# Kernel optimization log

Hardware: AMD Instinct MI355X
Metric: run time of the kernel (lower is better)

The kernel has to match this reference:

```python
import jax, jax.numpy as jnp
import numpy as np

EPS_RMS = 1e-6
EPS_NORM = 1e-9


def rmsnorm(x):
    return x * jax.lax.rsqrt(jnp.mean(x * x, axis=-1, keepdims=True) + EPS_RMS)


def apply_rotary(x, cos, sin):
    # x: [b, h, s, d]; cos/sin: [1, 1, s, d//2]
    d2 = x.shape[-1] // 2
    x1, x2 = x[..., :d2], x[..., d2:]
    return jnp.concatenate([x1 * cos - x2 * sin, x1 * sin + x2 * cos], axis=-1)


def setup_inputs() -> dict:
    key = jax.random.key(0)
    ks = jax.random.split(key, 16)
    b, l, e, h = 4, 1024, 2048, 16
    d = e // h
    query = jax.random.normal(ks[0], (b, l, e), jnp.float32)
    keyt = jax.random.normal(ks[1], (b, l, e), jnp.float32)
    value = jax.random.normal(ks[2], (b, l, e), jnp.float32)
    attn_mask = jnp.tril(jnp.ones((l, l), bool))[None, None]  # causal bool mask
    cos = jax.random.normal(ks[3], (1, 1, l, d // 2), jnp.float32)
    sin = jax.random.normal(ks[4], (1, 1, l, d // 2), jnp.float32)
    sc = 0.02
    Wq = jax.random.normal(ks[5], (e, e), jnp.float32) * sc
    bq = jnp.zeros((e,), jnp.float32)
    Wk = jax.random.normal(ks[6], (e, e), jnp.float32) * sc
    bk = jnp.zeros((e,), jnp.float32)
    Wv = jax.random.normal(ks[7], (e, e), jnp.float32) * sc
    bv = jnp.zeros((e,), jnp.float32)
    Wo = jax.random.normal(ks[8], (e, e), jnp.float32) * sc
    bo = jnp.zeros((e,), jnp.float32)
    return dict(query=query, key=keyt, value=value, attn_mask=attn_mask,
                cos=cos, sin=sin, Wq=Wq, bq=bq, Wk=Wk, bk=bk,
                Wv=Wv, bv=bv, Wo=Wo, bo=bo)


def reference(query, key, value, attn_mask, cos, sin, Wq, bq, Wk, bk, Wv, bv, Wo, bo):
    b, l, e = query.shape
    s = key.shape[1]
    h = 16
    d = e // h
    q = (query @ Wq.T + bq).reshape(b, l, h, d).transpose(0, 2, 1, 3)
    k = (key @ Wk.T + bk).reshape(b, s, h, d).transpose(0, 2, 1, 3)
    v = (value @ Wv.T + bv).reshape(b, s, h, d).transpose(0, 2, 1, 3)
    q, k = rmsnorm(q), rmsnorm(k)
    # rotary (self-attention, s == l)
    q = apply_rotary(q, cos[:, :, :s], sin[:, :, :s])
    k = apply_rotary(k, cos[:, :, :s], sin[:, :, :s])
    # SDPA with boolean mask
    scores = jnp.einsum('bhld,bhsd->bhls', q, k) / jnp.sqrt(jnp.float32(d))
    scores = jnp.where(attn_mask, scores, jnp.finfo(scores.dtype).min)
    p = jax.nn.softmax(scores, axis=-1)
    o = jnp.einsum('bhls,bhsd->bhld', p, v)  # [b,h,l,d]
    # post-attention v-orthogonalization (o.shape == v.shape here)
    vnorm = jnp.sqrt(jnp.sum(v * v, axis=-1, keepdims=True))
    vn = v / jnp.maximum(vnorm, EPS_NORM)
    o = o - jnp.sum(o * vn, axis=-1, keepdims=True) * vn
    o = o.transpose(0, 2, 1, 3).reshape(b, l, e)
    return o @ Wo.T + bo
```

## Files before the change

### kernel.cpp

```cpp
#include <hip/hip_runtime.h>

typedef short short8 __attribute__((ext_vector_type(8)));
typedef short short4v __attribute__((ext_vector_type(4)));
typedef float f32x4 __attribute__((ext_vector_type(4)));

#define MFMA_BF16 __builtin_amdgcn_mfma_f32_16x16x32_bf16

__device__ __forceinline__ unsigned short f2bf(float f) {
  unsigned int u = __float_as_uint(f);
  u += 0x7fffu + ((u >> 16) & 1u);
  return (unsigned short)(u >> 16);
}
__device__ __forceinline__ float bf2f(unsigned short u) {
  return __uint_as_float(((unsigned int)u) << 16);
}

typedef __attribute__((address_space(1))) const unsigned int as1_u32;
typedef __attribute__((address_space(3))) unsigned int as3_u32;
__device__ __forceinline__ void gld16(const void* g, void* l) {
  __builtin_amdgcn_global_load_lds((as1_u32*)(unsigned long long)g,
                                   (as3_u32*)(unsigned int)(unsigned long long)l,
                                   16, 0, 0);
}

template <int N>
__device__ __forceinline__ void vmwait() {
  if constexpr (N == 0) asm volatile("s_waitcnt vmcnt(0)" ::: "memory");
  else if constexpr (N == 4) asm volatile("s_waitcnt vmcnt(4)" ::: "memory");
  else if constexpr (N == 6) asm volatile("s_waitcnt vmcnt(6)" ::: "memory");
}
__device__ __forceinline__ void barrier_raw() {
  asm volatile("" ::: "memory");
  __builtin_amdgcn_s_barrier();
  asm volatile("" ::: "memory");
}

struct CvtArgs {
  const float* s[7];
  unsigned short* d[7];
  int n4[7];
};

__global__ __launch_bounds__(256) void cvtall(CvtArgs a) {
  const int seg = blockIdx.y;
  int i = blockIdx.x * 256 + threadIdx.x;
  if (i >= a.n4[seg]) return;
  const float4* s4 = (const float4*)a.s[seg];
  float4 x = s4[i];
  short4v o = {(short)f2bf(x.x), (short)f2bf(x.y), (short)f2bf(x.z), (short)f2bf(x.w)};
  *(short4v*)&a.d[seg][(size_t)i * 4] = o;
}

struct GemmArgs {
  const unsigned short* A[3];
  const unsigned short* W[3];
  const float* bias[3];
  unsigned short* Cb[3];
  float* Cf;
};

template <bool OUTBF, int NZ, int MF>
__global__ __launch_bounds__(256, 2) void gemm_bf16(GemmArgs g) {
  extern __shared__ unsigned short Sh[];
  constexpr int NA = MF / 2;
  constexpr int L = NA + 2;
  constexpr int MH = MF / 2;
  constexpr int BOFF = MF * 1024;
  constexpr int RS = MF * 1024 + 4096;
  const int K = 2048, N = 2048, NT = 64;

  const int B = blockIdx.x;
  int z, bm, bn;
  if constexpr (MF == 8) {
    z = B >> 8;
    const int i = B & 255;
    const int xcd = i & 7, q = i >> 3;
    bm = (xcd * 2 + (q & 1)) * 256;
    bn = (q >> 1) * 128;
  } else {
    z = 0;
    const int xcd = B & 7, q = B >> 3;
    bm = (xcd * 4 + (q & 3)) * 128;
    bn = (q >> 2) * 128;
  }

  const unsigned short* __restrict__ A = g.A[z];
  const unsigned short* __restrict__ W = g.W[z];
  const float* __restrict__ bias = g.bias[z];
  unsigned short* __restrict__ Cb = g.Cb[z];

  const int t = threadIdx.x, lane = t & 63, w = t >> 6;
  const int wr = w >> 1, wc = w & 1;
  const int quad = lane >> 4, l16 = lane & 15;

  const int sk = ((lane & 3) * 8) ^ (((lane >> 3) & 3) << 3);
  const int srow = lane >> 2;
  size_t gA[NA], gB[2];
  int lA[NA], lB[2];
  for (int j = 0; j < NA; ++j) {
    gA[j] = (size_t)(bm + w * (MF * 8) + j * 16 + srow) * K + sk;
    lA[j] = (w * (MF * 8) + j * 16) * 32;
  }
  for (int j = 0; j < 2; ++j) {
    gB[j] = (size_t)(bn + w * 32 + j * 16 + srow) * K + sk;
    lB[j] = BOFF + (w * 32 + j * 16) * 32;
  }

  auto STAGE_A = [&](int kq, unsigned short* Ld) {
    for (int j = 0; j < NA; ++j) gld16(A + gA[j] + kq, Ld + lA[j]);
  };
  auto STAGE_B = [&](int kq, unsigned short* Ld) {
    for (int j = 0; j < 2; ++j) gld16(W + gB[j] + kq, Ld + lB[j]);
  };

  const int ka = (quad * 8) ^ (((l16 >> 1) & 3) << 3);
  const int raA = (wr * (MF * 16) + l16) * 32 + ka;
  const int raB = BOFF + (wc * 64 + l16) * 32 + ka;

  const f32x4 fz = {0.f, 0.f, 0.f, 0.f};
  f32x4 acc[MF][4];
  for (int a = 0; a < MF; ++a)
    for (int b = 0; b < 4; ++b) acc[a][b] = fz;

  unsigned short* cur = Sh;
  unsigned short* nxt = Sh + RS;
  unsigned short* stg = Sh + 2 * RS;

  STAGE_A(0, cur);  STAGE_B(0, cur);
  STAGE_A(32, nxt); STAGE_B(32, nxt);
  vmwait<L>();
  barrier_raw();

  for (int tt = 0; tt < NT; ++tt) {
    short8 af0[MH], bv[4];
#pragma unroll
    for (int mt = 0; mt < MH; ++mt)
      af0[mt] = *(const short8*)&cur[raA + mt * 512];
#pragma unroll
    for (int nt = 0; nt < 4; ++nt)
      bv[nt] = *(const short8*)&cur[raB + nt * 512];
    if (tt + 2 < NT) STAGE_A((tt + 2) * 32, stg);
    barrier_raw();
    __builtin_amdgcn_s_setprio(1);
#pragma unroll
    for (int mt = 0; mt < MH; ++mt)
#pragma unroll
      for (int nt = 0; nt < 4; ++nt)
        acc[mt][nt] = MFMA_BF16(af0[mt], bv[nt], acc[mt][nt], 0, 0, 0);
    __builtin_amdgcn_s_setprio(0);
    barrier_raw();

    short8 af1[MH];
#pragma unroll
    for (int mt = 0; mt < MH; ++mt)
      af1[mt] = *(const short8*)&cur[raA + (MH + mt) * 512];
    if (tt + 2 < NT) STAGE_B((tt + 2) * 32, stg);
    if (tt < NT - 2) vmwait<L>();
    else if (tt == NT - 2) vmwait<0>();
    barrier_raw();
    __builtin_amdgcn_s_setprio(1);
#pragma unroll
    for (int mt = 0; mt < MH; ++mt)
#pragma unroll
      for (int nt = 0; nt < 4; ++nt)
        acc[MH + mt][nt] = MFMA_BF16(af1[mt], bv[nt], acc[MH + mt][nt], 0, 0, 0);
    __builtin_amdgcn_s_setprio(0);
    barrier_raw();

    unsigned short* tmp = cur; cur = nxt; nxt = stg; stg = tmp;
  }

  for (int mt = 0; mt < MF; ++mt)
    for (int nt = 0; nt < 4; ++nt) {
      int row = bm + wr * (MF * 16) + mt * 16 + quad * 4;
      int col = bn + wc * 64 + nt * 16 + l16;
      float bc = bias[col];
      for (int r2 = 0; r2 < 4; ++r2) {
        float v = acc[mt][nt][r2] + bc;
        if (OUTBF) Cb[(size_t)(row + r2) * N + col] = f2bf(v);
        else       g.Cf[(size_t)(row + r2) * N + col] = v;
      }
    }
}

__global__ __launch_bounds__(256) void rmsvt(
    const unsigned short* __restrict__ Qf, const unsigned short* __restrict__ Kf,
    const unsigned short* __restrict__ Vf,
    const float* __restrict__ cosT, const float* __restrict__ sinT,
    unsigned short* __restrict__ Qb, unsigned short* __restrict__ Kb,
    unsigned short* __restrict__ Vt) {
  __shared__ unsigned short Vsh[64 * 136];
  if (blockIdx.x < 16384) {
    const int rid = blockIdx.x * 4 + (threadIdx.x >> 6);
    const int lane = threadIdx.x & 63;
    const int li = rid & 1023;
    const int bh = rid >> 10;
    const int hi = bh & 15, bi = bh >> 4;
    const int src = (bi * 1024 + li) * 2048 + hi * 128;
    const int dst = rid * 128;
    const float c = cosT[li * 64 + lane];
    const float s = sinT[li * 64 + lane];

    float q1 = bf2f(Qf[src + lane]), q2 = bf2f(Qf[src + 64 + lane]);
    float ss = q1 * q1 + q2 * q2;
    for (int off = 32; off; off >>= 1) ss += __shfl_xor(ss, off, 64);
    float r = rsqrtf(ss * (1.f / 128.f) + 1e-6f);
    float qa = q1 * r, qb2 = q2 * r;
    const float qsc = 0.08838834764831845f * 1.4426950408889634f;
    Qb[dst + lane]      = f2bf((qa * c - qb2 * s) * qsc);
    Qb[dst + 64 + lane] = f2bf((qa * s + qb2 * c) * qsc);

    float k1 = bf2f(Kf[src + lane]), k2 = bf2f(Kf[src + 64 + lane]);
    float ks = k1 * k1 + k2 * k2;
    for (int off = 32; off; off >>= 1) ks += __shfl_xor(ks, off, 64);
    float rk = rsqrtf(ks * (1.f / 128.f) + 1e-6f);
    float ka = k1 * rk, kb2 = k2 * rk;
    Kb[dst + lane]      = f2bf(ka * c - kb2 * s);
    Kb[dst + 64 + lane] = f2bf(ka * s + kb2 * c);
  } else {
    const int bid = blockIdx.x - 16384;
    const int t = threadIdx.x;
    const int bh = bid >> 4, l0 = (bid & 15) * 64;
    const int hi = bh & 15, bi = bh >> 4;
    {
      int row = t >> 2, c4 = t & 3;
      const unsigned short* src = &Vf[(size_t)(bi * 1024 + l0 + row) * 2048 + hi * 128];
      for (int i = 0; i < 4; ++i) {
        int chunk = c4 * 4 + i;
        *(int4*)&Vsh[row * 136 + chunk * 8] = *(const int4*)&src[chunk * 8];
      }
    }
    __syncthreads();
    {
      int d = t >> 1, half = t & 1;
      unsigned short* dst = &Vt[(size_t)bh * 131072 + (size_t)d * 1024 + l0 + half * 32];
      for (int g = 0; g < 4; ++g) {
        short8 o;
        for (int j = 0; j < 8; ++j)
          o[j] = (short)Vsh[(half * 32 + g * 8 + j) * 136 + d];
        *(short8*)&dst[g * 8] = o;
      }
    }
  }
}

__global__ __launch_bounds__(512, 2) void attn(
    const unsigned short* __restrict__ Qb, const unsigned short* __restrict__ Kb,
    const unsigned short* __restrict__ Vt, unsigned short* __restrict__ Of0,
    unsigned short* __restrict__ Of1, float* __restrict__ Lb) {
  extern __shared__ unsigned short Sh[];
  const int t = threadIdx.x, lane = t & 63, w = t >> 6;
  const int quad = lane >> 4, l16 = lane & 15;
  const int B = blockIdx.x;
  const int bh = (B & 7) + 8 * ((B >> 3) & 7);
  const int p = (B >> 6) & 1, split = (B >> 7) & 1;
  const unsigned short* Qh = Qb + (size_t)bh * 131072;
  const unsigned short* Kh = Kb + (size_t)bh * 131072;
  const unsigned short* Vh = Vt + (size_t)bh * 131072;
  unsigned short* Oh = (split ? Of1 : Of0) + (size_t)bh * 131072;
  float* Lh = Lb + split * 65536 + bh * 1024;
  unsigned short* Pw = Sh + 32768 + w * 2304;

  const int kc = (lane & 15) * 8;
  const int vcc = (lane & 7) * 8;
  const f32x4 fz = {0.f, 0.f, 0.f, 0.f};

  auto STAGE = [&](int s0, int buf) {
    unsigned short* Kd = Sh + buf * 8192;
    unsigned short* Vd = Sh + 16384 + buf * 8192;
#pragma unroll
    for (int j = 0; j < 2; ++j) {
      int row = w * 8 + 4 * j + (lane >> 4);
      int sc = kc ^ ((row & 7) << 3);
      gld16(&Kh[(size_t)(s0 + row) * 128 + sc], &Kd[(w * 8 + 4 * j) * 128]);
    }
#pragma unroll
    for (int j = 0; j < 2; ++j) {
      int row = w * 16 + 8 * j + (lane >> 3);
      int sc = vcc ^ ((row & 7) << 3);
      gld16(&Vh[(size_t)row * 1024 + s0 + sc], &Vd[(w * 16 + 8 * j) * 64]);
    }
  };

  for (int ti = 0; ti < 2; ++ti) {
    const int qt = ti == 0 ? 3 - p : p;
    const int q0 = qt * 256;
    const int qw = q0 + w * 32;

    short8 aQ[2][4];
#pragma unroll
    for (int rt = 0; rt < 2; ++rt) {
      int qr = qw + rt * 16 + l16;
#pragma unroll
      for (int kk = 0; kk < 4; ++kk)
        aQ[rt][kk] = *(const short8*)&Qh[(size_t)qr * 128 + kk * 32 + quad * 8];
    }
    f32x4 oacc[2][8];
#pragma unroll
    for (int rt = 0; rt < 2; ++rt)
#pragma unroll
      for (int i = 0; i < 8; ++i) oacc[rt][i] = fz;
    float Lr[2][4] = {{0.f, 0.f, 0.f, 0.f}, {0.f, 0.f, 0.f, 0.f}};
    const int n = 2 * qt + 2;

    vmwait<0>();
    barrier_raw();
    STAGE(split * 64, 0);

    for (int i = 0; i < n; ++i) {
      const int s0 = (split + 2 * i) * 64;
      barrier_raw();
      if (i + 1 < n) {
        STAGE((split + 2 * (i + 1)) * 64, (i + 1) & 1);
        vmwait<4>();
      } else {
        vmwait<0>();
      }
      barrier_raw();
      const unsigned short* Kl = Sh + (i & 1) * 8192;
      const unsigned short* Vl = Sh + 16384 + (i & 1) * 8192;

      f32x4 sfr[2][4];
#pragma unroll
      for (int rt = 0; rt < 2; ++rt)
#pragma unroll
        for (int ni = 0; ni < 4; ++ni) sfr[rt][ni] = fz;
#pragma unroll
      for (int kk = 0; kk < 4; ++kk) {
        short8 bK[4];
#pragma unroll
        for (int ni = 0; ni < 4; ++ni)
          bK[ni] = *(const short8*)&Kl[(ni * 16 + l16) * 128 +
                                       ((kk * 32 + quad * 8) ^ ((l16 & 7) << 3))];
#pragma unroll
        for (int rt = 0; rt < 2; ++rt)
#pragma unroll
          for (int ni = 0; ni < 4; ++ni)
            sfr[rt][ni] = MFMA_BF16(aQ[rt][kk], bK[ni], sfr[rt][ni], 0, 0, 0);
      }

#pragma unroll
      for (int rt = 0; rt < 2; ++rt) {
        const bool diag = (s0 + 63 > qw + rt * 16);
#pragma unroll
        for (int r = 0; r < 4; ++r) {
          int q = qw + rt * 16 + quad * 4 + r;
          float ps = 0.f;
#pragma unroll
          for (int ni = 0; ni < 4; ++ni) {
            float sv = sfr[rt][ni][r];
            if (diag && (s0 + ni * 16 + l16 > q)) sv = -30000.f;
            float pp = exp2f(sv - 16.5f);
            ps += pp;
            Pw[(rt * 16 + quad * 4 + r) * 72 + ni * 16 + l16] = f2bf(pp);
          }
          ps += __shfl_xor(ps, 1, 64);
          ps += __shfl_xor(ps, 2, 64);
          ps += __shfl_xor(ps, 4, 64);
          ps += __shfl_xor(ps, 8, 64);
          Lr[rt][r] += ps;
        }
      }

#pragma unroll
      for (int kk = 0; kk < 2; ++kk) {
        short8 aP[2];
#pragma unroll
        for (int rt = 0; rt < 2; ++rt)
          aP[rt] = *(const short8*)&Pw[(rt * 16 + l16) * 72 + kk * 32 + quad * 8];
#pragma unroll
        for (int nt = 0; nt < 8; ++nt) {
          short8 bV = *(const short8*)&Vl[(nt * 16 + l16) * 64 +
                                          ((kk * 32 + quad * 8) ^ ((l16 & 7) << 3))];
#pragma unroll
          for (int rt = 0; rt < 2; ++rt)
            oacc[rt][nt] = MFMA_BF16(aP[rt], bV, oacc[rt][nt], 0, 0, 0);
        }
      }
    }

#pragma unroll
    for (int rt = 0; rt < 2; ++rt)
#pragma unroll
      for (int r = 0; r < 4; ++r) {
        int q = qw + rt * 16 + quad * 4 + r;
        size_t base = (size_t)q * 128;
#pragma unroll
        for (int nt = 0; nt < 8; ++nt)
          Oh[base + nt * 16 + l16] = f2bf(oacc[rt][nt][r]);
        if (l16 == 0) Lh[q] = Lr[rt][r];
      }
  }
}

__global__ __launch_bounds__(256) void vnfix(
    const unsigned short* __restrict__ Of0, const unsigned short* __restrict__ Of1,
    const float* __restrict__ Lb, const unsigned short* __restrict__ Vf,
    unsigned short* __restrict__ Op) {
  const int rid = blockIdx.x * 4 + (threadIdx.x >> 6);
  const int lane = threadIdx.x & 63;
  const int li = rid & 1023;
  const int bh = rid >> 10;
  const int hi = bh & 15, bi = bh >> 4;
  const int src = (bi * 1024 + li) * 2048 + hi * 128;
  float inv = 1.f / (Lb[rid] + Lb[65536 + rid]);
  float o1 = (bf2f(Of0[(size_t)rid * 128 + lane]) + bf2f(Of1[(size_t)rid * 128 + lane])) * inv;
  float o2 = (bf2f(Of0[(size_t)rid * 128 + 64 + lane]) + bf2f(Of1[(size_t)rid * 128 + 64 + lane])) * inv;
  float v1 = bf2f(Vf[src + lane]), v2 = bf2f(Vf[src + 64 + lane]);
  float vv = v1 * v1 + v2 * v2;
  float dd = o1 * v1 + o2 * v2;
  for (int off = 32; off; off >>= 1) {
    vv += __shfl_xor(vv, off, 64);
    dd += __shfl_xor(dd, off, 64);
  }
  float vn = fmaxf(sqrtf(vv), 1e-9f);
  float tc = dd / (vn * vn);
  Op[src + lane]      = f2bf(o1 - tc * v1);
  Op[src + 64 + lane] = f2bf(o2 - tc * v2);
}

extern "C" void kernel_launch(void* const* d_in, const int* in_sizes, int n_in,
                              void* d_out, int out_size, void* d_ws, size_t ws_size,
                              hipStream_t stream) {
  const float* query = (const float*)d_in[0];
  const float* key   = (const float*)d_in[1];
  const float* value = (const float*)d_in[2];
  const float* cosT  = (const float*)d_in[4];
  const float* sinT  = (const float*)d_in[5];
  const float* Wq = (const float*)d_in[6];
  const float* bq = (const float*)d_in[7];
  const float* Wk = (const float*)d_in[8];
  const float* bk = (const float*)d_in[9];
  const float* Wv = (const float*)d_in[10];
  const float* bv = (const float*)d_in[11];
  const float* Wo = (const float*)d_in[12];
  const float* bo = (const float*)d_in[13];
  float* out = (float*)d_out;

  char* ws = (char*)d_ws;
  const size_t MB = 1048576;
  unsigned short* Xq  = (unsigned short*)(ws);
  unsigned short* Xk  = (unsigned short*)(ws + 16 * MB);
  unsigned short* Xv  = (unsigned short*)(ws + 32 * MB);
  unsigned short* Wqb = (unsigned short*)(ws + 48 * MB);
  unsigned short* Wkb = (unsigned short*)(ws + 56 * MB);
  unsigned short* Wvb = (unsigned short*)(ws + 64 * MB);
  unsigned short* Wob = (unsigned short*)(ws + 72 * MB);
  unsigned short* Qf  = (unsigned short*)(ws + 80 * MB);
  unsigned short* Kf  = (unsigned short*)(ws + 96 * MB);
  unsigned short* Vf  = (unsigned short*)(ws + 112 * MB);
  unsigned short* Qbb = Xq;
  unsigned short* Kbb = Xk;
  unsigned short* Vtb = Xv;
  unsigned short* Of0 = Qf;
  unsigned short* Of1 = Kf;
  float*          Lbp = (float*)(ws + 64 * MB);
  unsigned short* Opb = (unsigned short*)(ws + 48 * MB);

  CvtArgs ca;
  ca.s[0] = query; ca.d[0] = Xq;  ca.n4[0] = 2097152;
  ca.s[1] = key;   ca.d[1] = Xk;  ca.n4[1] = 2097152;
  ca.s[2] = value; ca.d[2] = Xv;  ca.n4[2] = 2097152;
  ca.s[3] = Wq;    ca.d[3] = Wqb; ca.n4[3] = 1048576;
  ca.s[4] = Wk;    ca.d[4] = Wkb; ca.n4[4] = 1048576;
  ca.s[5] = Wv;    ca.d[5] = Wvb; ca.n4[5] = 1048576;
  ca.s[6] = Wo;    ca.d[6] = Wob; ca.n4[6] = 1048576;
  cvtall<<<dim3(8192, 7), 256, 0, stream>>>(ca);

  GemmArgs gp;
  gp.A[0] = Xq;  gp.A[1] = Xk;  gp.A[2] = Xv;
  gp.W[0] = Wqb; gp.W[1] = Wkb; gp.W[2] = Wvb;
  gp.bias[0] = bq; gp.bias[1] = bk; gp.bias[2] = bv;
  gp.Cb[0] = Qf; gp.Cb[1] = Kf; gp.Cb[2] = Vf;
  gp.Cf = nullptr;
  gemm_bf16<true, 3, 8><<<768, 256, 73728, stream>>>(gp);

  rmsvt<<<17408, 256, 0, stream>>>(Qf, Kf, Vf, cosT, sinT, Qbb, Kbb, Vtb);

  attn<<<256, 512, 102400, stream>>>(Qbb, Kbb, Vtb, Of0, Of1, Lbp);

  vnfix<<<16384, 256, 0, stream>>>(Of0, Of1, Lbp, Vf, Opb);

  GemmArgs go;
  go.A[0] = Opb; go.A[1] = nullptr; go.A[2] = nullptr;
  go.W[0] = Wob; go.W[1] = nullptr; go.W[2] = nullptr;
  go.bias[0] = bo; go.bias[1] = nullptr; go.bias[2] = nullptr;
  go.Cb[0] = nullptr; go.Cb[1] = nullptr; go.Cb[2] = nullptr;
  go.Cf = out;
  gemm_bf16<false, 1, 8><<<256, 256, 73728, stream>>>(go);
}
```

Measured before the change: 434.4 us.

## Fuse v-orthogonalization into attention and drop KV split for 128-row query tiles

Attention blocks now process 128-row query tiles (16 rows per wave) over the full key range instead of 256-row tiles with a two-way key split. Because each block holds the full softmax sum, the normalization and v-orthogonalization are done in the epilogue, which removes the separate vnfix kernel and the partial-output and partial-sum buffers in global memory. The causal mask is applied only on diagonal tiles, and shared memory for P shrinks. In exchange each wave does fewer MFMAs per K/V load, so data reuse drops, and per-block work is less evenly balanced across the grid.

```diff
diff --git a/kernel.cpp b/kernel.cpp
--- a/kernel.cpp
+++ b/kernel.cpp
@@ -246,20 +246,19 @@
 
 __global__ __launch_bounds__(512, 2) void attn(
     const unsigned short* __restrict__ Qb, const unsigned short* __restrict__ Kb,
-    const unsigned short* __restrict__ Vt, unsigned short* __restrict__ Of0,
-    unsigned short* __restrict__ Of1, float* __restrict__ Lb) {
+    const unsigned short* __restrict__ Vt, const unsigned short* __restrict__ Vf,
+    unsigned short* __restrict__ Op) {
   extern __shared__ unsigned short Sh[];
   const int t = threadIdx.x, lane = t & 63, w = t >> 6;
   const int quad = lane >> 4, l16 = lane & 15;
   const int B = blockIdx.x;
   const int bh = (B & 7) + 8 * ((B >> 3) & 7);
-  const int p = (B >> 6) & 1, split = (B >> 7) & 1;
+  const int p = B >> 6;
+  const int hi = bh & 15, bi = bh >> 4;
   const unsigned short* Qh = Qb + (size_t)bh * 131072;
   const unsigned short* Kh = Kb + (size_t)bh * 131072;
   const unsigned short* Vh = Vt + (size_t)bh * 131072;
-  unsigned short* Oh = (split ? Of1 : Of0) + (size_t)bh * 131072;
-  float* Lh = Lb + split * 65536 + bh * 1024;
-  unsigned short* Pw = Sh + 32768 + w * 2304;
+  unsigned short* Pw = Sh + 32768 + w * 1152;
 
   const int kc = (lane & 15) * 8;
   const int vcc = (lane & 7) * 8;
@@ -283,35 +282,31 @@
   };
 
   for (int ti = 0; ti < 2; ++ti) {
-    const int qt = ti == 0 ? 3 - p : p;
-    const int q0 = qt * 256;
-    const int qw = q0 + w * 32;
-
-    short8 aQ[2][4];
-#pragma unroll
-    for (int rt = 0; rt < 2; ++rt) {
-      int qr = qw + rt * 16 + l16;
+    const int qt = ti == 0 ? 7 - p : p;
+    const int qw = qt * 128 + w * 16;
+
+    short8 aQ[4];
+    {
+      int qr = qw + l16;
 #pragma unroll
       for (int kk = 0; kk < 4; ++kk)
-        aQ[rt][kk] = *(const short8*)&Qh[(size_t)qr * 128 + kk * 32 + quad * 8];
-    }
-    f32x4 oacc[2][8];
-#pragma unroll
-    for (int rt = 0; rt < 2; ++rt)
-#pragma unroll
-      for (int i = 0; i < 8; ++i) oacc[rt][i] = fz;
-    float Lr[2][4] = {{0.f, 0.f, 0.f, 0.f}, {0.f, 0.f, 0.f, 0.f}};
+        aQ[kk] = *(const short8*)&Qh[(size_t)qr * 128 + kk * 32 + quad * 8];
+    }
+    f32x4 oacc[8];
+#pragma unroll
+    for (int i = 0; i < 8; ++i) oacc[i] = fz;
+    float Lr[4] = {0.f, 0.f, 0.f, 0.f};
     const int n = 2 * qt + 2;
 
     vmwait<0>();
     barrier_raw();
-    STAGE(split * 64, 0);
+    STAGE(0, 0);
 
     for (int i = 0; i < n; ++i) {
-      const int s0 = (split + 2 * i) * 64;
+      const int s0 = i * 64;
       barrier_raw();
       if (i + 1 < n) {
-        STAGE((split + 2 * (i + 1)) * 64, (i + 1) & 1);
+        STAGE((i + 1) * 64, (i + 1) & 1);
         vmwait<4>();
       } else {
         vmwait<0>();
@@ -320,103 +315,92 @@
       const unsigned short* Kl = Sh + (i & 1) * 8192;
       const unsigned short* Vl = Sh + 16384 + (i & 1) * 8192;
 
-      f32x4 sfr[2][4];
-#pragma unroll
-      for (int rt = 0; rt < 2; ++rt)
-#pragma unroll
-        for (int ni = 0; ni < 4; ++ni) sfr[rt][ni] = fz;
-#pragma unroll
-      for (int kk = 0; kk < 4; ++kk) {
-        short8 bK[4];
-#pragma unroll
-        for (int ni = 0; ni < 4; ++ni)
-          bK[ni] = *(const short8*)&Kl[(ni * 16 + l16) * 128 +
-                                       ((kk * 32 + quad * 8) ^ ((l16 & 7) << 3))];
-#pragma unroll
-        for (int rt = 0; rt < 2; ++rt)
-#pragma unroll
-          for (int ni = 0; ni < 4; ++ni)
-            sfr[rt][ni] = MFMA_BF16(aQ[rt][kk], bK[ni], sfr[rt][ni], 0, 0, 0);
-      }
-
-#pragma unroll
-      for (int rt = 0; rt < 2; ++rt) {
-        const bool diag = (s0 + 63 > qw + rt * 16);
+      f32x4 sfr[4];
+#pragma unroll
+      for (int j = 0; j < 4; ++j) sfr[j] = fz;
+#pragma unroll
+      for (int kk = 0; kk < 4; ++kk)
+#pragma unroll
+        for (int ni = 0; ni < 4; ++ni) {
+          short8 bK = *(const short8*)&Kl[(ni * 16 + l16) * 128 +
+                                          ((kk * 32 + quad * 8) ^ ((l16 & 7) << 3))];
+          sfr[ni] = MFMA_BF16(aQ[kk], bK, sfr[ni], 0, 0, 0);
+        }
+
+      if (i >= 2 * qt) {
 #pragma unroll
         for (int r = 0; r < 4; ++r) {
-          int q = qw + rt * 16 + quad * 4 + r;
+          int q = qw + quad * 4 + r;
           float ps = 0.f;
 #pragma unroll
           for (int ni = 0; ni < 4; ++ni) {
-            float sv = sfr[rt][ni][r];
-            if (diag && (s0 + ni * 16 + l16 > q)) sv = -30000.f;
+            float sv = sfr[ni][r];
+            if (s0 + ni * 16 + l16 > q) sv = -30000.f;
             float pp = exp2f(sv - 16.5f);
             ps += pp;
-            Pw[(rt * 16 + quad * 4 + r) * 72 + ni * 16 + l16] = f2bf(pp);
+            Pw[(quad * 4 + r) * 72 + ni * 16 + l16] = f2bf(pp);
           }
           ps += __shfl_xor(ps, 1, 64);
           ps += __shfl_xor(ps, 2, 64);
           ps += __shfl_xor(ps, 4, 64);
           ps += __shfl_xor(ps, 8, 64);
-          Lr[rt][r] += ps;
+          Lr[r] += ps;
         }
+      } else {
+#pragma unroll
+        for (int r = 0; r < 4; ++r) {
+          float ps = 0.f;
+#pragma unroll
+          for (int ni = 0; ni < 4; ++ni) {
+            float pp = exp2f(sfr[ni][r] - 16.5f);
+            ps += pp;
+            Pw[(quad * 4 + r) * 72 + ni * 16 + l16] = f2bf(pp);
+          }
+          ps += __shfl_xor(ps, 1, 64);
+          ps += __shfl_xor(ps, 2, 64);
+          ps += __shfl_xor(ps, 4, 64);
+          ps += __shfl_xor(ps, 8, 64);
+          Lr[r] += ps;
+        }
       }
 
 #pragma unroll
       for (int kk = 0; kk < 2; ++kk) {
-        short8 aP[2];
-#pragma unroll
-        for (int rt = 0; rt < 2; ++rt)
-          aP[rt] = *(const short8*)&Pw[(rt * 16 + l16) * 72 + kk * 32 + quad * 8];
+        short8 aP = *(const short8*)&Pw[l16 * 72 + kk * 32 + quad * 8];
 #pragma unroll
         for (int nt = 0; nt < 8; ++nt) {
           short8 bV = *(const short8*)&Vl[(nt * 16 + l16) * 64 +
                                           ((kk * 32 + quad * 8) ^ ((l16 & 7) << 3))];
-#pragma unroll
-          for (int rt = 0; rt < 2; ++rt)
-            oacc[rt][nt] = MFMA_BF16(aP[rt], bV, oacc[rt][nt], 0, 0, 0);
+          oacc[nt] = MFMA_BF16(aP, bV, oacc[nt], 0, 0, 0);
         }
       }
     }
 
 #pragma unroll
-    for (int rt = 0; rt < 2; ++rt)
-#pragma unroll
-      for (int r = 0; r < 4; ++r) {
-        int q = qw + rt * 16 + quad * 4 + r;
-        size_t base = (size_t)q * 128;
-#pragma unroll
-        for (int nt = 0; nt < 8; ++nt)
-          Oh[base + nt * 16 + l16] = f2bf(oacc[rt][nt][r]);
-        if (l16 == 0) Lh[q] = Lr[rt][r];
-      }
-  }
-}
-
-__global__ __launch_bounds__(256) void vnfix(
-    const unsigned short* __restrict__ Of0, const unsigned short* __restrict__ Of1,
-    const float* __restrict__ Lb, const unsigned short* __restrict__ Vf,
-    unsigned short* __restrict__ Op) {
-  const int rid = blockIdx.x * 4 + (threadIdx.x >> 6);
-  const int lane = threadIdx.x & 63;
-  const int li = rid & 1023;
-  const int bh = rid >> 10;
-  const int hi = bh & 15, bi = bh >> 4;
-  const int src = (bi * 1024 + li) * 2048 + hi * 128;
-  float inv = 1.f / (Lb[rid] + Lb[65536 + rid]);
-  float o1 = (bf2f(Of0[(size_t)rid * 128 + lane]) + bf2f(Of1[(size_t)rid * 128 + lane])) * inv;
-  float o2 = (bf2f(Of0[(size_t)rid * 128 + 64 + lane]) + bf2f(Of1[(size_t)rid * 128 + 64 + lane])) * inv;
-  float v1 = bf2f(Vf[src + lane]), v2 = bf2f(Vf[src + 64 + lane]);
-  float vv = v1 * v1 + v2 * v2;
-  float dd = o1 * v1 + o2 * v2;
-  for (int off = 32; off; off >>= 1) {
-    vv += __shfl_xor(vv, off, 64);
-    dd += __shfl_xor(dd, off, 64);
-  }
-  float vn = fmaxf(sqrtf(vv), 1e-9f);
-  float tc = dd / (vn * vn);
-  Op[src + lane]      = f2bf(o1 - tc * v1);
-  Op[src + 64 + lane] = f2bf(o2 - tc * v2);
+    for (int r = 0; r < 4; ++r) {
+      int q = qw + quad * 4 + r;
+      float inv = 1.f / Lr[r];
+      const unsigned short* vrow = &Vf[((size_t)(bi * 1024 + q)) * 2048 + hi * 128];
+      float vr[8], vv = 0.f, dd = 0.f;
+#pragma unroll
+      for (int nt = 0; nt < 8; ++nt) {
+        vr[nt] = bf2f(vrow[nt * 16 + l16]);
+        vv += vr[nt] * vr[nt];
+        dd += oacc[nt][r] * vr[nt];
+      }
+#pragma unroll
+      for (int off = 1; off < 16; off <<= 1) {
+        vv += __shfl_xor(vv, off, 64);
+        dd += __shfl_xor(dd, off, 64);
+      }
+      dd *= inv;
+      float tc = dd / fmaxf(vv, 1e-18f);
+      unsigned short* orow = &Op[((size_t)(bi * 1024 + q)) * 2048 + hi * 128];
+#pragma unroll
+      for (int nt = 0; nt < 8; ++nt)
+        orow[nt * 16 + l16] = f2bf(oacc[nt][r] * inv - tc * vr[nt]);
+    }
+  }
 }
 
 extern "C" void kernel_launch(void* const* d_in, const int* in_sizes, int n_in,
@@ -452,9 +436,6 @@
   unsigned short* Qbb = Xq;
   unsigned short* Kbb = Xk;
   unsigned short* Vtb = Xv;
-  unsigned short* Of0 = Qf;
-  unsigned short* Of1 = Kf;
-  float*          Lbp = (float*)(ws + 64 * MB);
   unsigned short* Opb = (unsigned short*)(ws + 48 * MB);
 
   CvtArgs ca;
@@ -477,9 +458,7 @@
 
   rmsvt<<<17408, 256, 0, stream>>>(Qf, Kf, Vf, cosT, sinT, Qbb, Kbb, Vtb);
 
-  attn<<<256, 512, 102400, stream>>>(Qbb, Kbb, Vtb, Of0, Of1, Lbp);
-
-  vnfix<<<16384, 256, 0, stream>>>(Of0, Of1, Lbp, Vf, Opb);
+  attn<<<256, 512, 83968, stream>>>(Qbb, Kbb, Vtb, Vf, Opb);
 
   GemmArgs go;
   go.A[0] = Opb; go.A[1] = nullptr; go.A[2] = nullptr;
```

After: 412.4 us. -5.1%, faster.
